# Optimization experiments

Hardware: AMD Instinct MI355X
Metric: run time of the kernel (lower is better)

The kernel has to match this reference:

```python
import jax, jax.numpy as jnp
import numpy as np

B, S, D_MODEL, N_HEADS, D_FEAT = 8, 1024, 1024, 16, 64


def setup_inputs() -> dict:
    key = jax.random.key(0)
    ks = jax.random.split(key, 5)
    sin = jax.random.normal(ks[0], (B, S, D_MODEL), dtype=jnp.float32)
    mask = jnp.ones((B, S), dtype=bool)  # only its presence matters in the original
    # Per-head Linear(d_model -> d_feature): weight stored as [H, d_model, d_feature]
    lim = 1.0 / np.sqrt(D_MODEL)
    Wx = jax.random.uniform(ks[1], (N_HEADS, D_MODEL, D_FEAT), dtype=jnp.float32, minval=-lim, maxval=lim)
    bx = jax.random.uniform(ks[2], (N_HEADS, D_FEAT), dtype=jnp.float32, minval=-lim, maxval=lim)
    # Output projection Linear(H*d_feature -> d_model), stored as [in, out]
    lim_p = 1.0 / np.sqrt(N_HEADS * D_FEAT)
    Wp = jax.random.uniform(ks[3], (N_HEADS * D_FEAT, D_MODEL), dtype=jnp.float32, minval=-lim_p, maxval=lim_p)
    bp = jax.random.uniform(ks[4], (D_MODEL,), dtype=jnp.float32, minval=-lim_p, maxval=lim_p)
    return {"sin": sin, "mask": mask, "Wx": Wx, "bx": bx, "Wp": Wp, "bp": bp}


def reference(sin, mask, Wx, bx, Wp, bp):
    # All heads batched: per-head linear projection  [B,H,S,F]
    x = jnp.einsum("bsd,hdf->bhsf", sin, Wx) + bx[None, :, None, :]
    # Cosine-similarity scores: x x^T / (||x|| ||x||^T)  -> [B,H,S,S]
    norm = jnp.sqrt(jnp.sum(x * x, axis=-1, keepdims=True))  # [B,H,S,1]
    scores = jnp.einsum("bhsf,bhtf->bhst", x, x) / (norm * jnp.swapaxes(norm, -2, -1))
    # Original quirk: when mask is not None, entries that are exactly 0.0 get -inf
    scores = jnp.where(scores == 0.0, -jnp.inf, scores)
    p_attn = jax.nn.softmax(scores, axis=-1)
    out = jnp.einsum("bhst,bhtf->bhsf", p_attn, x)
    # Concat heads: [B,S,H*F]
    out = jnp.transpose(out, (0, 2, 1, 3)).reshape(out.shape[0], out.shape[2], -1)
    return out @ Wp + bp
```

## Files before the change

kernel.cpp:

```cpp
#include <hip/hip_runtime.h>
#include <hip/hip_bf16.h>
#include <math.h>

typedef _Float16 f16;
typedef _Float16 half8 __attribute__((ext_vector_type(8)));
typedef float f32x4 __attribute__((ext_vector_type(4)));

#define NB 8
#define NS 1024
#define DM 1024
#define NH 16
#define NF 64

__global__ __launch_bounds__(256) void csin_kernel(const float* __restrict__ in, f16* __restrict__ out) {
  long gid = (long)blockIdx.x * 256 + threadIdx.x;
  const float4* p = (const float4*)(in + gid * 8);
  float4 a = p[0], b = p[1];
  half8 v;
  v[0] = (f16)a.x; v[1] = (f16)a.y; v[2] = (f16)a.z; v[3] = (f16)a.w;
  v[4] = (f16)b.x; v[5] = (f16)b.y; v[6] = (f16)b.z; v[7] = (f16)b.w;
  *(half8*)(out + gid * 8) = v;
}

__global__ __launch_bounds__(256) void cwx_kernel(const float* __restrict__ Wx, f16* __restrict__ W2T) {
  int gid = blockIdx.x * 256 + threadIdx.x;
  int n = gid >> 7;
  int d0 = (gid & 127) * 8;
  const float* src = Wx + (n >> 6) * (DM * NF) + (n & 63);
  half8 v;
#pragma unroll
  for (int j = 0; j < 8; ++j) v[j] = (f16)src[(size_t)(d0 + j) * NF];
  *(half8*)(W2T + (size_t)n * DM + d0) = v;
}

__global__ __launch_bounds__(256) void cwp_kernel(const float* __restrict__ Wp, f16* __restrict__ WpT) {
  int gid = blockIdx.x * 256 + threadIdx.x;
  int n = gid >> 7;
  int d0 = (gid & 127) * 8;
  const float* src = Wp + n;
  half8 v;
#pragma unroll
  for (int j = 0; j < 8; ++j) v[j] = (f16)src[(size_t)(d0 + j) * DM];
  *(half8*)(WpT + (size_t)n * DM + d0) = v;
}

template <int MODE>
__global__ __launch_bounds__(256) void gemm_kernel(const f16* __restrict__ A, const f16* __restrict__ Bt,
                                                   const float* __restrict__ bias, void* __restrict__ Cv) {
  __shared__ f16 As[128][72];
  __shared__ f16 Bs[128][72];
  int tid = threadIdx.x;
  int l = tid & 63, wv = tid >> 6;
  int wm = wv >> 1, wn = wv & 1;
  int bm = blockIdx.x >> 3, bn = blockIdx.x & 7;
  int lr = l & 15, lh = l >> 4;

  f32x4 acc[4][4];
#pragma unroll
  for (int i = 0; i < 4; ++i)
#pragma unroll
    for (int j = 0; j < 4; ++j) acc[i][j] = (f32x4)0.f;

  for (int k0 = 0; k0 < DM; k0 += 64) {
    __syncthreads();
#pragma unroll
    for (int c = 0; c < 4; ++c) {
      int idx = c * 256 + tid;
      int row = idx >> 3, ch = idx & 7;
      *(half8*)&As[row][ch * 8] = *(const half8*)(A + (size_t)(bm * 128 + row) * DM + k0 + ch * 8);
      *(half8*)&Bs[row][ch * 8] = *(const half8*)(Bt + (size_t)(bn * 128 + row) * DM + k0 + ch * 8);
    }
    __syncthreads();
#pragma unroll
    for (int ks = 0; ks < 2; ++ks) {
      half8 af[4], bf[4];
#pragma unroll
      for (int mi = 0; mi < 4; ++mi) af[mi] = *(const half8*)&As[wm * 64 + mi * 16 + lr][ks * 32 + lh * 8];
#pragma unroll
      for (int ni = 0; ni < 4; ++ni) bf[ni] = *(const half8*)&Bs[wn * 64 + ni * 16 + lr][ks * 32 + lh * 8];
#pragma unroll
      for (int mi = 0; mi < 4; ++mi)
#pragma unroll
        for (int ni = 0; ni < 4; ++ni)
          acc[mi][ni] = __builtin_amdgcn_mfma_f32_16x16x32_f16(af[mi], bf[ni], acc[mi][ni], 0, 0, 0);
    }
  }

#pragma unroll
  for (int mi = 0; mi < 4; ++mi)
#pragma unroll
    for (int ni = 0; ni < 4; ++ni) {
      int gc = bn * 128 + wn * 64 + ni * 16 + lr;
      float bv = bias[gc];
#pragma unroll
      for (int r = 0; r < 4; ++r) {
        int gr = bm * 128 + wm * 64 + mi * 16 + lh * 4 + r;
        float v = acc[mi][ni][r] + bv;
        if (MODE == 0) {
          f16* x = (f16*)Cv;
          int b = gr >> 10, s = gr & 1023, h = gc >> 6, f = gc & 63;
          x[(size_t)((b * NH + h) * NS + s) * NF + f] = (f16)v;
        } else {
          ((float*)Cv)[(size_t)gr * DM + gc] = v;
        }
      }
    }
}

__global__ __launch_bounds__(256) void norm_kernel(const f16* __restrict__ x, float* __restrict__ invn) {
  int gid = blockIdx.x * 256 + threadIdx.x;
  int row = gid >> 2, sub = gid & 3;
  const f16* p = x + (size_t)row * NF + sub * 16;
  half8 a = *(const half8*)p;
  half8 b = *(const half8*)(p + 8);
  float ss = 0.f;
#pragma unroll
  for (int i = 0; i < 8; ++i) {
    float u = (float)a[i], w = (float)b[i];
    ss += u * u + w * w;
  }
  ss += __shfl_xor(ss, 1, 64);
  ss += __shfl_xor(ss, 2, 64);
  if (sub == 0) invn[row] = 1.0f / sqrtf(ss);
}

__global__ __launch_bounds__(256) void attn_kernel(const f16* __restrict__ x, const float* __restrict__ invn,
                                                   f16* __restrict__ ao) {
  __shared__ f16 Xk[128][72];
  __shared__ f16 XkT[64][136];
  __shared__ f16 P[128][136];
  __shared__ float sn[NS];

  int tid = threadIdx.x;
  int l = tid & 63, wv = tid >> 6;
  int lr = l & 15, lh = l >> 4;
  int bh = blockIdx.x >> 3, q0 = (blockIdx.x & 7) * 128;
  const f16* xb = x + (size_t)bh * (NS * NF);

  for (int i = tid; i < NS; i += 256) sn[i] = invn[bh * NS + i];

  int wq = wv * 32;
  half8 aq[2][2];
#pragma unroll
  for (int mi = 0; mi < 2; ++mi)
#pragma unroll
    for (int ks = 0; ks < 2; ++ks)
      aq[mi][ks] = *(const half8*)(xb + (size_t)(q0 + wq + mi * 16 + lr) * NF + ks * 32 + lh * 8);

  __syncthreads();
  float qn_[2][4];
#pragma unroll
  for (int mi = 0; mi < 2; ++mi)
#pragma unroll
    for (int r = 0; r < 4; ++r) qn_[mi][r] = sn[q0 + wq + mi * 16 + lh * 4 + r];

  f32x4 accO[2][4];
  float rs[2][4];
#pragma unroll
  for (int mi = 0; mi < 2; ++mi) {
#pragma unroll
    for (int ni = 0; ni < 4; ++ni) accO[mi][ni] = (f32x4)0.f;
#pragma unroll
    for (int r = 0; r < 4; ++r) rs[mi][r] = 0.f;
  }

  for (int t0 = 0; t0 < NS; t0 += 128) {
    __syncthreads();
#pragma unroll
    for (int c = 0; c < 4; ++c) {
      int idx = c * 256 + tid;
      int tr = idx >> 3, fo = (idx & 7) * 8;
      half8 v = *(const half8*)(xb + (size_t)(t0 + tr) * NF + fo);
      *(half8*)&Xk[tr][fo] = v;
#pragma unroll
      for (int j = 0; j < 8; ++j) XkT[fo + j][tr] = v[j];
    }
    __syncthreads();

    f32x4 s[2][8];
#pragma unroll
    for (int mi = 0; mi < 2; ++mi)
#pragma unroll
      for (int ni = 0; ni < 8; ++ni) s[mi][ni] = (f32x4)0.f;
#pragma unroll
    for (int ks = 0; ks < 2; ++ks) {
      half8 bk[8];
#pragma unroll
      for (int ni = 0; ni < 8; ++ni) bk[ni] = *(const half8*)&Xk[ni * 16 + lr][ks * 32 + lh * 8];
#pragma unroll
      for (int mi = 0; mi < 2; ++mi)
#pragma unroll
        for (int ni = 0; ni < 8; ++ni)
          s[mi][ni] = __builtin_amdgcn_mfma_f32_16x16x32_f16(aq[mi][ks], bk[ni], s[mi][ni], 0, 0, 0);
    }

#pragma unroll
    for (int ni = 0; ni < 8; ++ni) {
      float kn = sn[t0 + ni * 16 + lr];
#pragma unroll
      for (int mi = 0; mi < 2; ++mi)
#pragma unroll
        for (int r = 0; r < 4; ++r) {
          float sv = s[mi][ni][r] * qn_[mi][r] * kn;
          float e = (sv == 0.f) ? 0.f : __expf(sv - 1.f);
          rs[mi][r] += e;
          P[wq + mi * 16 + lh * 4 + r][ni * 16 + lr] = (f16)e;
        }
    }

#pragma unroll
    for (int ks = 0; ks < 4; ++ks) {
      half8 pa[2], vb[4];
#pragma unroll
      for (int mi = 0; mi < 2; ++mi) pa[mi] = *(const half8*)&P[wq + mi * 16 + lr][ks * 32 + lh * 8];
#pragma unroll
      for (int ni = 0; ni < 4; ++ni) vb[ni] = *(const half8*)&XkT[ni * 16 + lr][ks * 32 + lh * 8];
#pragma unroll
      for (int mi = 0; mi < 2; ++mi)
#pragma unroll
        for (int ni = 0; ni < 4; ++ni)
          accO[mi][ni] = __builtin_amdgcn_mfma_f32_16x16x32_f16(pa[mi], vb[ni], accO[mi][ni], 0, 0, 0);
    }
  }

#pragma unroll
  for (int mi = 0; mi < 2; ++mi)
#pragma unroll
    for (int r = 0; r < 4; ++r) {
      float v = rs[mi][r];
      v += __shfl_xor(v, 1, 64);
      v += __shfl_xor(v, 2, 64);
      v += __shfl_xor(v, 4, 64);
      v += __shfl_xor(v, 8, 64);
      rs[mi][r] = v;
    }

  int b = bh >> 4, h = bh & 15;
#pragma unroll
  for (int mi = 0; mi < 2; ++mi)
#pragma unroll
    for (int ni = 0; ni < 4; ++ni)
#pragma unroll
      for (int r = 0; r < 4; ++r) {
        int s_g = q0 + wq + mi * 16 + lh * 4 + r;
        int f = ni * 16 + lr;
        float v = accO[mi][ni][r] / rs[mi][r];
        ao[(size_t)(b * NS + s_g) * DM + h * NF + f] = (f16)v;
      }
}

extern "C" void kernel_launch(void* const* d_in, const int* in_sizes, int n_in,
                              void* d_out, int out_size, void* d_ws, size_t ws_size,
                              hipStream_t stream) {
  const float* sin_in = (const float*)d_in[0];
  const float* Wx = (const float*)d_in[2];
  const float* bx = (const float*)d_in[3];
  const float* Wp = (const float*)d_in[4];
  const float* bp = (const float*)d_in[5];
  float* out = (float*)d_out;

  char* p = (char*)d_ws;
  f16* sinb = (f16*)p;                      p += (size_t)NB * NS * DM * 2;
  f16* x    = (f16*)p;                      p += (size_t)NB * NH * NS * NF * 2;
  f16* ao   = (f16*)p;                      p += (size_t)NB * NS * DM * 2;
  f16* W2T  = (f16*)p;                      p += (size_t)DM * DM * 2;
  f16* WpT  = (f16*)p;                      p += (size_t)DM * DM * 2;
  float* invn = (float*)p;

  csin_kernel<<<4096, 256, 0, stream>>>(sin_in, sinb);
  cwx_kernel<<<512, 256, 0, stream>>>(Wx, W2T);
  cwp_kernel<<<512, 256, 0, stream>>>(Wp, WpT);
  gemm_kernel<0><<<512, 256, 0, stream>>>(sinb, W2T, bx, (void*)x);
  norm_kernel<<<2048, 256, 0, stream>>>(x, invn);
  attn_kernel<<<1024, 256, 0, stream>>>(x, invn, ao);
  gemm_kernel<1><<<512, 256, 0, stream>>>(ao, WpT, bp, (void*)out);
}
```

Measured before the change: 265.7 us.

## Rewrite attention to register-resident P with 32x32 MFMA and direct global-to-LDS GEMM loads

The GEMM now stages tiles with global_load_lds, writing global data straight into unpadded LDS. A new transpose kernel writes an unnormalized xT for the value operand. The norm kernel now normalizes x in place. The attention kernel drops shared memory and barriers entirely: it uses 32x32x16 MFMAs, keeps P in registers via lane shuffles, and reads K and V tiles directly from global/L2. The aim is to remove LDS traffic, the per-element scaling and the synchronization in attention, at the cost of an extra transpose pass and uncached repeated global reads. The unpadded LDS tiles may also cause bank conflicts in the GEMM.

Result: slower. 299.3 us (+12.7%).

```diff
diff --git a/kernel.cpp b/kernel.cpp
--- a/kernel.cpp
+++ b/kernel.cpp
@@ -5,6 +5,8 @@
 typedef _Float16 f16;
 typedef _Float16 half8 __attribute__((ext_vector_type(8)));
 typedef float f32x4 __attribute__((ext_vector_type(4)));
+typedef float f32x16 __attribute__((ext_vector_type(16)));
+typedef unsigned int u32;
 
 #define NB 8
 #define NS 1024
@@ -47,8 +49,8 @@
 template <int MODE>
 __global__ __launch_bounds__(256) void gemm_kernel(const f16* __restrict__ A, const f16* __restrict__ Bt,
                                                    const float* __restrict__ bias, void* __restrict__ Cv) {
-  __shared__ f16 As[128][72];
-  __shared__ f16 Bs[128][72];
+  __shared__ f16 As[128][64];
+  __shared__ f16 Bs[128][64];
   int tid = threadIdx.x;
   int l = tid & 63, wv = tid >> 6;
   int wm = wv >> 1, wn = wv & 1;
@@ -61,14 +63,21 @@
 #pragma unroll
     for (int j = 0; j < 4; ++j) acc[i][j] = (f32x4)0.f;
 
+  const f16* gA = A + (size_t)(bm * 128 + wv * 32 + (l >> 3)) * DM + (l & 7) * 8;
+  const f16* gB = Bt + (size_t)(bn * 128 + wv * 32 + (l >> 3)) * DM + (l & 7) * 8;
+  f16* ldsA = &As[wv * 32][0];
+  f16* ldsB = &Bs[wv * 32][0];
+
   for (int k0 = 0; k0 < DM; k0 += 64) {
     __syncthreads();
 #pragma unroll
     for (int c = 0; c < 4; ++c) {
-      int idx = c * 256 + tid;
-      int row = idx >> 3, ch = idx & 7;
-      *(half8*)&As[row][ch * 8] = *(const half8*)(A + (size_t)(bm * 128 + row) * DM + k0 + ch * 8);
-      *(half8*)&Bs[row][ch * 8] = *(const half8*)(Bt + (size_t)(bn * 128 + row) * DM + k0 + ch * 8);
+      __builtin_amdgcn_global_load_lds(
+          (const __attribute__((address_space(1))) void*)(gA + k0 + (size_t)c * 8 * DM),
+          (__attribute__((address_space(3))) void*)(ldsA + c * 512), 16, 0, 0);
+      __builtin_amdgcn_global_load_lds(
+          (const __attribute__((address_space(1))) void*)(gB + k0 + (size_t)c * 8 * DM),
+          (__attribute__((address_space(3))) void*)(ldsB + c * 512), 16, 0, 0);
     }
     __syncthreads();
 #pragma unroll
@@ -107,10 +116,34 @@
     }
 }
 
-__global__ __launch_bounds__(256) void norm_kernel(const f16* __restrict__ x, float* __restrict__ invn) {
+__global__ __launch_bounds__(256) void transx_kernel(const f16* __restrict__ x, f16* __restrict__ xT) {
+  __shared__ f16 T[64][64];
+  int bh = blockIdx.x >> 4, s0 = (blockIdx.x & 15) * 64;
+  int tid = threadIdx.x;
+  const f16* xb = x + (size_t)bh * (NS * NF);
+#pragma unroll
+  for (int it = 0; it < 2; ++it) {
+    int idx = it * 256 + tid;
+    int sr = idx >> 3, fcb = idx & 7;
+    half8 v = *(const half8*)(xb + (size_t)(s0 + sr) * NF + fcb * 8);
+    *(half8*)&T[sr][((fcb ^ ((sr >> 3) & 7)) * 8)] = v;
+  }
+  __syncthreads();
+#pragma unroll
+  for (int it = 0; it < 2; ++it) {
+    int idx = it * 256 + tid;
+    int fr = idx >> 3, scb = idx & 7;
+    half8 v;
+#pragma unroll
+    for (int j = 0; j < 8; ++j) v[j] = T[scb * 8 + j][(((fr >> 3) ^ scb) * 8) + (fr & 7)];
+    *(half8*)(xT + ((size_t)bh * NF + fr) * NS + s0 + scb * 8) = v;
+  }
+}
+
+__global__ __launch_bounds__(256) void normx_kernel(f16* __restrict__ x) {
   int gid = blockIdx.x * 256 + threadIdx.x;
   int row = gid >> 2, sub = gid & 3;
-  const f16* p = x + (size_t)row * NF + sub * 16;
+  f16* p = x + (size_t)row * NF + sub * 16;
   half8 a = *(const half8*)p;
   half8 b = *(const half8*)(p + 8);
   float ss = 0.f;
@@ -121,132 +154,101 @@
   }
   ss += __shfl_xor(ss, 1, 64);
   ss += __shfl_xor(ss, 2, 64);
-  if (sub == 0) invn[row] = 1.0f / sqrtf(ss);
-}
-
-__global__ __launch_bounds__(256) void attn_kernel(const f16* __restrict__ x, const float* __restrict__ invn,
+  float inv = rsqrtf(ss);
+  half8 an, bn;
+#pragma unroll
+  for (int i = 0; i < 8; ++i) {
+    an[i] = (f16)((float)a[i] * inv);
+    bn[i] = (f16)((float)b[i] * inv);
+  }
+  *(half8*)p = an;
+  *(half8*)(p + 8) = bn;
+}
+
+__global__ __launch_bounds__(256) void attn_kernel(const f16* __restrict__ xn, const f16* __restrict__ xT,
                                                    f16* __restrict__ ao) {
-  __shared__ f16 Xk[128][72];
-  __shared__ f16 XkT[64][136];
-  __shared__ f16 P[128][136];
-  __shared__ float sn[NS];
-
   int tid = threadIdx.x;
   int l = tid & 63, wv = tid >> 6;
-  int lr = l & 15, lh = l >> 4;
+  int lq = l & 31, hi = l >> 5;
+  int kq = hi * 8;
   int bh = blockIdx.x >> 3, q0 = (blockIdx.x & 7) * 128;
-  const f16* xb = x + (size_t)bh * (NS * NF);
-
-  for (int i = tid; i < NS; i += 256) sn[i] = invn[bh * NS + i];
-
-  int wq = wv * 32;
-  half8 aq[2][2];
-#pragma unroll
-  for (int mi = 0; mi < 2; ++mi)
-#pragma unroll
-    for (int ks = 0; ks < 2; ++ks)
-      aq[mi][ks] = *(const half8*)(xb + (size_t)(q0 + wq + mi * 16 + lr) * NF + ks * 32 + lh * 8);
-
-  __syncthreads();
-  float qn_[2][4];
-#pragma unroll
-  for (int mi = 0; mi < 2; ++mi)
-#pragma unroll
-    for (int r = 0; r < 4; ++r) qn_[mi][r] = sn[q0 + wq + mi * 16 + lh * 4 + r];
-
-  f32x4 accO[2][4];
-  float rs[2][4];
-#pragma unroll
-  for (int mi = 0; mi < 2; ++mi) {
-#pragma unroll
-    for (int ni = 0; ni < 4; ++ni) accO[mi][ni] = (f32x4)0.f;
-#pragma unroll
-    for (int r = 0; r < 4; ++r) rs[mi][r] = 0.f;
-  }
+  const f16* xnb = xn + (size_t)bh * (NS * NF);
+  const f16* xTb = xT + (size_t)bh * (NF * NS);
+
+  int q = q0 + wv * 32 + lq;
+
+  half8 bq[4];
+#pragma unroll
+  for (int ks = 0; ks < 4; ++ks)
+    bq[ks] = *(const half8*)(xnb + (size_t)q * NF + ks * 16 + kq);
+
+  f32x16 accO[2];
+  accO[0] = (f32x16)0.f;
+  accO[1] = (f32x16)0.f;
+  float rs = 0.f;
 
   for (int t0 = 0; t0 < NS; t0 += 128) {
-    __syncthreads();
-#pragma unroll
-    for (int c = 0; c < 4; ++c) {
-      int idx = c * 256 + tid;
-      int tr = idx >> 3, fo = (idx & 7) * 8;
-      half8 v = *(const half8*)(xb + (size_t)(t0 + tr) * NF + fo);
-      *(half8*)&Xk[tr][fo] = v;
-#pragma unroll
-      for (int j = 0; j < 8; ++j) XkT[fo + j][tr] = v[j];
-    }
-    __syncthreads();
-
-    f32x4 s[2][8];
-#pragma unroll
-    for (int mi = 0; mi < 2; ++mi)
-#pragma unroll
-      for (int ni = 0; ni < 8; ++ni) s[mi][ni] = (f32x4)0.f;
-#pragma unroll
-    for (int ks = 0; ks < 2; ++ks) {
-      half8 bk[8];
-#pragma unroll
-      for (int ni = 0; ni < 8; ++ni) bk[ni] = *(const half8*)&Xk[ni * 16 + lr][ks * 32 + lh * 8];
-#pragma unroll
-      for (int mi = 0; mi < 2; ++mi)
-#pragma unroll
-        for (int ni = 0; ni < 8; ++ni)
-          s[mi][ni] = __builtin_amdgcn_mfma_f32_16x16x32_f16(aq[mi][ks], bk[ni], s[mi][ni], 0, 0, 0);
-    }
-
-#pragma unroll
-    for (int ni = 0; ni < 8; ++ni) {
-      float kn = sn[t0 + ni * 16 + lr];
-#pragma unroll
-      for (int mi = 0; mi < 2; ++mi)
-#pragma unroll
-        for (int r = 0; r < 4; ++r) {
-          float sv = s[mi][ni][r] * qn_[mi][r] * kn;
-          float e = (sv == 0.f) ? 0.f : __expf(sv - 1.f);
-          rs[mi][r] += e;
-          P[wq + mi * 16 + lh * 4 + r][ni * 16 + lr] = (f16)e;
+#pragma unroll
+    for (int ti = 0; ti < 4; ++ti) {
+      f32x16 sa = (f32x16)0.f;
+      int tr = t0 + ti * 32 + lq;
+#pragma unroll
+      for (int ks = 0; ks < 4; ++ks) {
+        half8 ak = *(const half8*)(xnb + (size_t)tr * NF + ks * 16 + kq);
+        sa = __builtin_amdgcn_mfma_f32_32x32x16_f16(ak, bq[ks], sa, 0, 0, 0);
+      }
+      u32 pk[8];
+#pragma unroll
+      for (int m = 0; m < 8; ++m) {
+        float a = sa[2 * m], b = sa[2 * m + 1];
+        float ea = (a == 0.f) ? 0.f : __expf(a - 1.f);
+        float eb = (b == 0.f) ? 0.f : __expf(b - 1.f);
+        rs += ea + eb;
+        auto h = __builtin_amdgcn_cvt_pkrtz(ea, eb);
+        pk[m] = __builtin_bit_cast(u32, h);
+      }
+      u32 sw[8];
+#pragma unroll
+      for (int m = 0; m < 8; ++m) sw[m] = (u32)__shfl_xor((int)pk[m], 32, 64);
+      bool lo = (hi == 0);
+      uint4 a0, a1;
+      a0.x = lo ? pk[0] : sw[2];
+      a0.y = lo ? pk[1] : sw[3];
+      a0.z = lo ? sw[0] : pk[2];
+      a0.w = lo ? sw[1] : pk[3];
+      a1.x = lo ? pk[4] : sw[6];
+      a1.y = lo ? pk[5] : sw[7];
+      a1.z = lo ? sw[4] : pk[6];
+      a1.w = lo ? sw[5] : pk[7];
+      half8 pa0 = __builtin_bit_cast(half8, a0);
+      half8 pa1 = __builtin_bit_cast(half8, a1);
+#pragma unroll
+      for (int sub = 0; sub < 2; ++sub) {
+        half8 pa = sub ? pa1 : pa0;
+#pragma unroll
+        for (int ni = 0; ni < 2; ++ni) {
+          half8 vb = *(const half8*)(xTb + (size_t)(ni * 32 + lq) * NS + t0 + ti * 32 + sub * 16 + kq);
+          accO[ni] = __builtin_amdgcn_mfma_f32_32x32x16_f16(pa, vb, accO[ni], 0, 0, 0);
         }
-    }
-
-#pragma unroll
-    for (int ks = 0; ks < 4; ++ks) {
-      half8 pa[2], vb[4];
-#pragma unroll
-      for (int mi = 0; mi < 2; ++mi) pa[mi] = *(const half8*)&P[wq + mi * 16 + lr][ks * 32 + lh * 8];
-#pragma unroll
-      for (int ni = 0; ni < 4; ++ni) vb[ni] = *(const half8*)&XkT[ni * 16 + lr][ks * 32 + lh * 8];
-#pragma unroll
-      for (int mi = 0; mi < 2; ++mi)
-#pragma unroll
-        for (int ni = 0; ni < 4; ++ni)
-          accO[mi][ni] = __builtin_amdgcn_mfma_f32_16x16x32_f16(pa[mi], vb[ni], accO[mi][ni], 0, 0, 0);
-    }
-  }
-
-#pragma unroll
-  for (int mi = 0; mi < 2; ++mi)
-#pragma unroll
-    for (int r = 0; r < 4; ++r) {
-      float v = rs[mi][r];
-      v += __shfl_xor(v, 1, 64);
-      v += __shfl_xor(v, 2, 64);
-      v += __shfl_xor(v, 4, 64);
-      v += __shfl_xor(v, 8, 64);
-      rs[mi][r] = v;
-    }
+      }
+    }
+  }
+
+  rs += __shfl_xor(rs, 32, 64);
 
   int b = bh >> 4, h = bh & 15;
 #pragma unroll
-  for (int mi = 0; mi < 2; ++mi)
-#pragma unroll
-    for (int ni = 0; ni < 4; ++ni)
-#pragma unroll
-      for (int r = 0; r < 4; ++r) {
-        int s_g = q0 + wq + mi * 16 + lh * 4 + r;
-        int f = ni * 16 + lr;
-        float v = accO[mi][ni][r] / rs[mi][r];
-        ao[(size_t)(b * NS + s_g) * DM + h * NF + f] = (f16)v;
-      }
+  for (int r = 0; r < 16; ++r) {
+    int qoff = (r & 3) + 8 * (r >> 2) + 4 * hi;
+    float rv = __shfl(rs, qoff, 64);
+    float rinv = 1.0f / rv;
+    int qg = q0 + wv * 32 + qoff;
+#pragma unroll
+    for (int ni = 0; ni < 2; ++ni) {
+      int f = ni * 32 + lq;
+      ao[((size_t)(b * NS + qg)) * DM + h * NF + f] = (f16)(accO[ni][r] * rinv);
+    }
+  }
 }
 
 extern "C" void kernel_launch(void* const* d_in, const int* in_sizes, int n_in,
@@ -262,16 +264,17 @@
   char* p = (char*)d_ws;
   f16* sinb = (f16*)p;                      p += (size_t)NB * NS * DM * 2;
   f16* x    = (f16*)p;                      p += (size_t)NB * NH * NS * NF * 2;
-  f16* ao   = (f16*)p;                      p += (size_t)NB * NS * DM * 2;
+  f16* xT   = (f16*)p;                      p += (size_t)NB * NH * NF * NS * 2;
   f16* W2T  = (f16*)p;                      p += (size_t)DM * DM * 2;
   f16* WpT  = (f16*)p;                      p += (size_t)DM * DM * 2;
-  float* invn = (float*)p;
+  f16* ao   = sinb;
 
   csin_kernel<<<4096, 256, 0, stream>>>(sin_in, sinb);
   cwx_kernel<<<512, 256, 0, stream>>>(Wx, W2T);
   cwp_kernel<<<512, 256, 0, stream>>>(Wp, WpT);
   gemm_kernel<0><<<512, 256, 0, stream>>>(sinb, W2T, bx, (void*)x);
-  norm_kernel<<<2048, 256, 0, stream>>>(x, invn);
-  attn_kernel<<<1024, 256, 0, stream>>>(x, invn, ao);
+  transx_kernel<<<2048, 256, 0, stream>>>(x, xT);
+  normx_kernel<<<2048, 256, 0, stream>>>(x);
+  attn_kernel<<<1024, 256, 0, stream>>>(x, xT, ao);
   gemm_kernel<1><<<512, 256, 0, stream>>>(ao, WpT, bp, (void*)out);
 }
```
